# Kernel tuning notes

Hardware: AMD Instinct MI355X
Metric: run time of the kernel (lower is better)

## Reference

```python
import jax, jax.numpy as jnp
import numpy as np

INPUT_DIM = 20000
UNITS = 4096
NNZ = 2_000_000
BATCH = 2048


def setup_inputs() -> dict:
    key = jax.random.key(0)
    k1, k2, k3, k4 = jax.random.split(key, 4)
    x = jax.random.normal(k1, (BATCH, INPUT_DIM), dtype=jnp.float32)
    kernel_vector = jax.random.normal(k2, (NNZ,), dtype=jnp.float32) * 0.05
    bias = jnp.zeros((UNITS,), dtype=jnp.float32)
    rows = jax.random.randint(k3, (NNZ,), 0, INPUT_DIM, dtype=jnp.int32)
    cols = jax.random.randint(k4, (NNZ,), 0, UNITS, dtype=jnp.int32)
    nonzero_ind = jnp.stack([rows, cols], axis=1)  # (NNZ, 2)
    return {"x": x, "kernel_vector": kernel_vector, "bias": bias, "nonzero_ind": nonzero_ind}


def reference(x, kernel_vector, bias, nonzero_ind):
    # scatter_nd: build dense (input_dim, units) kernel from COO representation.
    # Duplicate indices accumulate (tf.scatter_nd semantics) -> use .add.
    trans = jnp.zeros((INPUT_DIM, UNITS), dtype=kernel_vector.dtype)
    trans = trans.at[nonzero_ind[:, 0], nonzero_ind[:, 1]].add(kernel_vector)
    out = x @ trans + bias  # (batch, units)
    return jnp.tanh(out)
```

## Files before the change

kernel.cpp:

```cpp
#include <hip/hip_runtime.h>
#include <cstdint>
#include <cstddef>

#define M_DIM 2048
#define N_DIM 4096
#define K_DIM 20000
#define KP    20480
#define KZ    10240
#define NTILE 160
#define WBT_BYTES  167772160UL
#define XB_OFFSET  167772160UL
#define CP_OFFSET  251658240UL
#define BIN_OFFSET CP_OFFSET
#define CUR_OFFSET 318767104UL
#define NBUCKET 256
#define BUCKET_CAP 16384
#define LDS_ECAP 9216

typedef __attribute__((ext_vector_type(8))) short short8;
typedef __attribute__((ext_vector_type(4))) float float4v;
typedef __attribute__((ext_vector_type(8))) unsigned short ushort8;

__device__ __forceinline__ unsigned short f2bf_rne(float f) {
    union { float f; unsigned int u; } v; v.f = f;
    unsigned int u = v.u;
    u += 0x7FFFu + ((u >> 16) & 1u);
    return (unsigned short)(u >> 16);
}

__device__ __forceinline__ void gload_lds16(const void* g, void* l) {
    __builtin_amdgcn_global_load_lds(
        (const __attribute__((address_space(1))) void*)g,
        (__attribute__((address_space(3))) void*)l, 16, 0, 0);
}

__global__ __launch_bounds__(256) void bin_kernel(
    const float* __restrict__ kv, const int* __restrict__ ind, int nnz,
    uint2* __restrict__ binned, unsigned int* __restrict__ cursor) {
    __shared__ unsigned int hist[NBUCKET];
    __shared__ unsigned int base[NBUCKET];
    __shared__ unsigned int run[NBUCKET];
    const int tid = threadIdx.x;
    const int per_block = (nnz + 1023) >> 10;
    const int start = blockIdx.x * per_block;
    const int limit = min(per_block, nnz - start);

    hist[tid] = 0u;
    __syncthreads();

    int bkt[8]; unsigned int meta[8]; float val[8];
    #pragma unroll
    for (int i = 0; i < 8; ++i) {
        int j = i * 256 + tid;
        bkt[i] = -1;
        if (j < limit) {
            int idx = start + j;
            int r = ind[2 * idx];
            int c = ind[2 * idx + 1];
            val[i] = kv[idx];
            bkt[i] = c >> 4;
            meta[i] = ((unsigned int)(c & 15) << 16) | (unsigned int)r;
            atomicAdd(&hist[bkt[i]], 1u);
        }
    }
    __syncthreads();
    {
        unsigned int n = hist[tid];
        base[tid] = n ? atomicAdd(&cursor[tid * 16], n) : 0u;
        run[tid] = 0u;
    }
    __syncthreads();
    #pragma unroll
    for (int i = 0; i < 8; ++i) {
        if (bkt[i] >= 0) {
            unsigned int slot = base[bkt[i]] + atomicAdd(&run[bkt[i]], 1u);
            if (slot < BUCKET_CAP) {
                uint2 e; e.x = meta[i]; e.y = __float_as_uint(val[i]);
                binned[(size_t)bkt[i] * BUCKET_CAP + slot] = e;
            }
        }
    }
}

__global__ __launch_bounds__(512) void accum_kernel(
    const uint2* __restrict__ binned, const unsigned int* __restrict__ cursor,
    unsigned short* __restrict__ Wbt) {
    __shared__ float row[KP];
    __shared__ uint2 ent[LDS_ECAP];
    const int b   = blockIdx.x;
    const int tid = threadIdx.x;
    const unsigned int count = min(cursor[b * 16], (unsigned int)BUCKET_CAP);
    const uint2* gsrc = binned + (size_t)b * BUCKET_CAP;

    for (unsigned int i = tid; i < count && i < LDS_ECAP; i += 512)
        ent[i] = gsrc[i];
    __syncthreads();

    for (int cc = 0; cc < 16; ++cc) {
        float4v* r4 = (float4v*)row;
        #pragma unroll
        for (int i = 0; i < 10; ++i)
            r4[tid + i * 512] = (float4v){0.f, 0.f, 0.f, 0.f};
        __syncthreads();
        for (unsigned int i = tid; i < count; i += 512) {
            uint2 e = (i < LDS_ECAP) ? ent[i] : gsrc[i];
            if ((int)(e.x >> 16) == cc)
                atomicAdd(&row[e.x & 0xFFFFu], __uint_as_float(e.y));
        }
        __syncthreads();
        unsigned short* dst = Wbt + (size_t)(b * 16 + cc) * KP;
        #pragma unroll
        for (int i = 0; i < 10; ++i) {
            int ch = tid + i * 512;
            float4v f = *(float4v*)&row[ch * 4];
            ushort4 o;
            o.x = f2bf_rne(f[0]); o.y = f2bf_rne(f[1]);
            o.z = f2bf_rne(f[2]); o.w = f2bf_rne(f[3]);
            *(ushort4*)(dst + ch * 4) = o;
        }
        __syncthreads();
    }
}

__global__ void convert_kernel(const float* __restrict__ src,
                               unsigned short* __restrict__ dst) {
    size_t t = (size_t)blockIdx.x * 256 + threadIdx.x;
    int row = (int)(t / 2560);
    int c8  = (int)(t % 2560);
    ushort8 o;
    if (c8 < 2500) {
        const float4* sv = (const float4*)(src + (size_t)row * K_DIM + (size_t)c8 * 8);
        float4 a = sv[0];
        float4 b = sv[1];
        o[0] = f2bf_rne(a.x); o[1] = f2bf_rne(a.y);
        o[2] = f2bf_rne(a.z); o[3] = f2bf_rne(a.w);
        o[4] = f2bf_rne(b.x); o[5] = f2bf_rne(b.y);
        o[6] = f2bf_rne(b.z); o[7] = f2bf_rne(b.w);
    } else {
        o = (ushort8)0;
    }
    *(ushort8*)(dst + (size_t)row * KP + (size_t)c8 * 8) = o;
}

__global__ __launch_bounds__(512, 2) void gemm256_kernel(
    const unsigned short* __restrict__ A,
    const unsigned short* __restrict__ Bt,
    float* __restrict__ Cp) {

    __shared__ unsigned short L[65536];

    const int t    = threadIdx.x;
    const int w    = t >> 6;
    const int l    = t & 63;
    const int quad = l >> 4;
    const int r16  = l & 15;
    const int wm   = w >> 2;
    const int wn   = w & 3;

    const int m0 = blockIdx.y * 256;
    const int n0 = blockIdx.x * 256;
    const size_t k0 = (size_t)blockIdx.z * KZ;

    const int lr8 = l >> 3;
    const int sl  = (l & 7) ^ lr8;
    const int w1024 = w << 10;

    const unsigned short* pA0 = A  + (size_t)(m0 +   0 + w * 8 + lr8) * KP + k0 + sl * 8;
    const unsigned short* pA1 = A  + (size_t)(m0 +  64 + w * 8 + lr8) * KP + k0 + sl * 8;
    const unsigned short* pA2 = A  + (size_t)(m0 + 128 + w * 8 + lr8) * KP + k0 + sl * 8;
    const unsigned short* pA3 = A  + (size_t)(m0 + 192 + w * 8 + lr8) * KP + k0 + sl * 8;
    const unsigned short* pB0 = Bt + (size_t)(n0 +   0 + w * 8 + lr8) * KP + k0 + sl * 8;
    const unsigned short* pB1 = Bt + (size_t)(n0 +  64 + w * 8 + lr8) * KP + k0 + sl * 8;
    const unsigned short* pB2 = Bt + (size_t)(n0 + 128 + w * 8 + lr8) * KP + k0 + sl * 8;
    const unsigned short* pB3 = Bt + (size_t)(n0 + 192 + w * 8 + lr8) * KP + k0 + sl * 8;

    char* Lb = (char*)L;

#define STG_A(OB, Q, P) do { \
    gload_lds16(P, Lb + (OB) + (Q) * 8192 + w1024); P += 64; } while (0)
#define STG_B(OB, Q, P) do { \
    gload_lds16(P, Lb + (OB) + 32768 + (Q) * 8192 + w1024); P += 64; } while (0)

    const int h   = r16 & 7;
    const int so0 = ((quad ^ h) << 4);
    const int so1 = (((4 | quad) ^ h) << 4);
    const int aoff = wm * 16384 + r16 * 128;
    const int boff = 32768 + wn * 8192 + r16 * 128;

    float4v acc[8][4];
#pragma unroll
    for (int i = 0; i < 8; ++i)
#pragma unroll
        for (int j = 0; j < 4; ++j)
            acc[i][j] = (float4v){0.f, 0.f, 0.f, 0.f};

    short8 bfr[4], af[4];

#define VM2 asm volatile("s_waitcnt vmcnt(2)" ::: "memory")
#define VMNONE ((void)0)

#define PHASE(BUF, MH, SO, LOADB, STG, VM) do { \
    const char* base_ = Lb + (BUF); \
    if (LOADB) { \
        _Pragma("unroll") \
        for (int j = 0; j < 4; ++j) \
            bfr[j] = *(const short8*)(base_ + boff + j * 2048 + (SO)); \
    } \
    _Pragma("unroll") \
    for (int i = 0; i < 4; ++i) \
        af[i] = *(const short8*)(base_ + aoff + (MH) * 8192 + i * 2048 + (SO)); \
    STG; \
    __builtin_amdgcn_s_barrier(); \
    asm volatile("s_waitcnt lgkmcnt(0)" ::: "memory"); \
    __builtin_amdgcn_s_setprio(1); \
    _Pragma("unroll") \
    for (int i = 0; i < 4; ++i) \
        _Pragma("unroll") \
        for (int j = 0; j < 4; ++j) \
            acc[(MH) * 4 + i][j] = __builtin_amdgcn_mfma_f32_16x16x32_bf16( \
                af[i], bfr[j], acc[(MH) * 4 + i][j], 0, 0, 0); \
    __builtin_amdgcn_s_setprio(0); \
    VM; \
    __builtin_amdgcn_s_barrier(); \
} while (0)

#define TILE(BUF, OB) do { \
    PHASE(BUF, 0, so0, true,  { STG_A(OB, 0, pA0); STG_A(OB, 1, pA1); }, VMNONE); \
    PHASE(BUF, 1, so0, false, { STG_A(OB, 2, pA2); STG_A(OB, 3, pA3); }, VMNONE); \
    PHASE(BUF, 0, so1, true,  { STG_B(OB, 2, pB2); STG_B(OB, 3, pB3); }, VMNONE); \
    PHASE(BUF, 1, so1, false, { STG_B(BUF, 0, pB0); STG_B(BUF, 1, pB1); }, VM2); \
} while (0)

    STG_A(0, 0, pA0); STG_A(0, 1, pA1); STG_A(0, 2, pA2); STG_A(0, 3, pA3);
    STG_B(0, 0, pB0); STG_B(0, 1, pB1); STG_B(0, 2, pB2); STG_B(0, 3, pB3);
    STG_B(65536, 0, pB0); STG_B(65536, 1, pB1);
    asm volatile("s_waitcnt vmcnt(2)" ::: "memory");
    __builtin_amdgcn_s_barrier();

#pragma unroll 1
    for (int it = 0; it < NTILE / 2; ++it) {
        TILE(0, 65536);
        TILE(65536, 0);
    }
    asm volatile("s_waitcnt vmcnt(0)" ::: "memory");

    float* Cz = Cp + (size_t)blockIdx.z * ((size_t)M_DIM * N_DIM);
#pragma unroll
    for (int i = 0; i < 8; ++i) {
        const int row = m0 + wm * 128 + i * 16 + quad * 4;
#pragma unroll
        for (int j = 0; j < 4; ++j) {
            const int col = n0 + wn * 64 + j * 16 + r16;
#pragma unroll
            for (int r = 0; r < 4; ++r)
                Cz[(size_t)(row + r) * N_DIM + col] = acc[i][j][r];
        }
    }
#undef TILE
#undef PHASE
#undef STG_A
#undef STG_B
#undef VM2
#undef VMNONE
}

__global__ void combine_kernel(const float* __restrict__ Cp,
                               const float* __restrict__ bias,
                               float* __restrict__ out) {
    size_t t = (size_t)blockIdx.x * 256 + threadIdx.x;
    const size_t stride = (size_t)M_DIM * N_DIM / 4;
    float4 a = ((const float4*)Cp)[t];
    float4 b = ((const float4*)Cp)[t + stride];
    float4 bv = ((const float4*)bias)[t & (N_DIM / 4 - 1)];
    float4 o;
    o.x = tanhf(a.x + b.x + bv.x);
    o.y = tanhf(a.y + b.y + bv.y);
    o.z = tanhf(a.z + b.z + bv.z);
    o.w = tanhf(a.w + b.w + bv.w);
    ((float4*)out)[t] = o;
}

extern "C" void kernel_launch(void* const* d_in, const int* in_sizes, int n_in,
                              void* d_out, int out_size, void* d_ws, size_t ws_size,
                              hipStream_t stream) {
    const float* x    = (const float*)d_in[0];
    const float* kv   = (const float*)d_in[1];
    const float* bias = (const float*)d_in[2];
    const int*   ind  = (const int*)d_in[3];
    const int nnz = in_sizes[1];

    unsigned short* Wbt = (unsigned short*)d_ws;
    unsigned short* xb  = (unsigned short*)((char*)d_ws + XB_OFFSET);
    float* Cp           = (float*)((char*)d_ws + CP_OFFSET);
    uint2* binned       = (uint2*)((char*)d_ws + BIN_OFFSET);
    unsigned int* cursor = (unsigned int*)((char*)d_ws + CUR_OFFSET);

    hipMemsetAsync(cursor, 0, NBUCKET * 64, stream);
    bin_kernel<<<1024, 256, 0, stream>>>(kv, ind, nnz, binned, cursor);
    accum_kernel<<<NBUCKET, 512, 0, stream>>>(binned, cursor, Wbt);
    convert_kernel<<<(M_DIM * (KP / 8)) / 256, 256, 0, stream>>>(x, xb);
    gemm256_kernel<<<dim3(N_DIM / 256, M_DIM / 256, 2), 512, 0, stream>>>(
        xb, Wbt, Cp);
    combine_kernel<<<(M_DIM * N_DIM) / (256 * 4), 256, 0, stream>>>(
        Cp, bias, (float*)d_out);
}
```

Before: 613.9 us.

## Fuse x conversion into binning kernel and split accum buckets across two blocks

The bf16 conversion of x is merged into the COO binning kernel as extra blocks, which removes one launch and lets the conversion run alongside binning. The accumulation kernel now launches two blocks per bucket, each handling 8 of the 16 columns, which doubles the grid from 256 to 512 blocks on a GPU with many CUs. The LDS staging of bucket entries is dropped, so each block rereads its bucket from global memory once per column pass.

```diff
diff --git a/kernel.cpp b/kernel.cpp
--- a/kernel.cpp
+++ b/kernel.cpp
@@ -15,7 +15,8 @@
 #define CUR_OFFSET 318767104UL
 #define NBUCKET 256
 #define BUCKET_CAP 16384
-#define LDS_ECAP 9216
+#define BIN_BLOCKS 1024
+#define CONV_BLOCKS 20480
 
 typedef __attribute__((ext_vector_type(8))) short short8;
 typedef __attribute__((ext_vector_type(4))) float float4v;
@@ -34,81 +35,101 @@
         (__attribute__((address_space(3))) void*)l, 16, 0, 0);
 }
 
-__global__ __launch_bounds__(256) void bin_kernel(
+__global__ __launch_bounds__(256) void prep_kernel(
     const float* __restrict__ kv, const int* __restrict__ ind, int nnz,
-    uint2* __restrict__ binned, unsigned int* __restrict__ cursor) {
+    uint2* __restrict__ binned, unsigned int* __restrict__ cursor,
+    const float* __restrict__ x, unsigned short* __restrict__ xb) {
     __shared__ unsigned int hist[NBUCKET];
     __shared__ unsigned int base[NBUCKET];
     __shared__ unsigned int run[NBUCKET];
     const int tid = threadIdx.x;
-    const int per_block = (nnz + 1023) >> 10;
-    const int start = blockIdx.x * per_block;
-    const int limit = min(per_block, nnz - start);
-
-    hist[tid] = 0u;
-    __syncthreads();
-
-    int bkt[8]; unsigned int meta[8]; float val[8];
-    #pragma unroll
-    for (int i = 0; i < 8; ++i) {
-        int j = i * 256 + tid;
-        bkt[i] = -1;
-        if (j < limit) {
-            int idx = start + j;
-            int r = ind[2 * idx];
-            int c = ind[2 * idx + 1];
-            val[i] = kv[idx];
-            bkt[i] = c >> 4;
-            meta[i] = ((unsigned int)(c & 15) << 16) | (unsigned int)r;
-            atomicAdd(&hist[bkt[i]], 1u);
-        }
-    }
-    __syncthreads();
-    {
-        unsigned int n = hist[tid];
-        base[tid] = n ? atomicAdd(&cursor[tid * 16], n) : 0u;
-        run[tid] = 0u;
-    }
-    __syncthreads();
-    #pragma unroll
-    for (int i = 0; i < 8; ++i) {
-        if (bkt[i] >= 0) {
-            unsigned int slot = base[bkt[i]] + atomicAdd(&run[bkt[i]], 1u);
-            if (slot < BUCKET_CAP) {
-                uint2 e; e.x = meta[i]; e.y = __float_as_uint(val[i]);
-                binned[(size_t)bkt[i] * BUCKET_CAP + slot] = e;
+
+    if (blockIdx.x < BIN_BLOCKS) {
+        const int per_block = (nnz + BIN_BLOCKS - 1) / BIN_BLOCKS;
+        const int start = blockIdx.x * per_block;
+        const int limit = min(per_block, nnz - start);
+
+        hist[tid] = 0u;
+        __syncthreads();
+
+        int bkt[8]; unsigned int meta[8]; float val[8];
+        #pragma unroll
+        for (int i = 0; i < 8; ++i) {
+            int j = i * 256 + tid;
+            bkt[i] = -1;
+            if (j < limit) {
+                int idx = start + j;
+                int r = ind[2 * idx];
+                int c = ind[2 * idx + 1];
+                val[i] = kv[idx];
+                bkt[i] = c >> 4;
+                meta[i] = ((unsigned int)(c & 15) << 16) | (unsigned int)r;
+                atomicAdd(&hist[bkt[i]], 1u);
             }
         }
-    }
+        __syncthreads();
+        {
+            unsigned int n = hist[tid];
+            base[tid] = n ? atomicAdd(&cursor[tid * 16], n) : 0u;
+            run[tid] = 0u;
+        }
+        __syncthreads();
+        #pragma unroll
+        for (int i = 0; i < 8; ++i) {
+            if (bkt[i] >= 0) {
+                unsigned int slot = base[bkt[i]] + atomicAdd(&run[bkt[i]], 1u);
+                if (slot < BUCKET_CAP) {
+                    uint2 e; e.x = meta[i]; e.y = __float_as_uint(val[i]);
+                    binned[(size_t)bkt[i] * BUCKET_CAP + slot] = e;
+                }
+            }
+        }
+        return;
+    }
+
+    size_t t = (size_t)(blockIdx.x - BIN_BLOCKS) * 256 + tid;
+    int row = (int)(t / 2560);
+    int c8  = (int)(t % 2560);
+    ushort8 o;
+    if (c8 < 2500) {
+        const float4* sv = (const float4*)(x + (size_t)row * K_DIM + (size_t)c8 * 8);
+        float4 a = sv[0];
+        float4 b = sv[1];
+        o[0] = f2bf_rne(a.x); o[1] = f2bf_rne(a.y);
+        o[2] = f2bf_rne(a.z); o[3] = f2bf_rne(a.w);
+        o[4] = f2bf_rne(b.x); o[5] = f2bf_rne(b.y);
+        o[6] = f2bf_rne(b.z); o[7] = f2bf_rne(b.w);
+    } else {
+        o = (ushort8)0;
+    }
+    *(ushort8*)(xb + (size_t)row * KP + (size_t)c8 * 8) = o;
 }
 
 __global__ __launch_bounds__(512) void accum_kernel(
     const uint2* __restrict__ binned, const unsigned int* __restrict__ cursor,
     unsigned short* __restrict__ Wbt) {
     __shared__ float row[KP];
-    __shared__ uint2 ent[LDS_ECAP];
-    const int b   = blockIdx.x;
-    const int tid = threadIdx.x;
-    const unsigned int count = min(cursor[b * 16], (unsigned int)BUCKET_CAP);
-    const uint2* gsrc = binned + (size_t)b * BUCKET_CAP;
-
-    for (unsigned int i = tid; i < count && i < LDS_ECAP; i += 512)
-        ent[i] = gsrc[i];
-    __syncthreads();
-
-    for (int cc = 0; cc < 16; ++cc) {
+    const int b      = blockIdx.x;
+    const int bucket = b >> 1;
+    const int half   = b & 1;
+    const int tid    = threadIdx.x;
+    const unsigned int count = min(cursor[bucket * 16], (unsigned int)BUCKET_CAP);
+    const uint2* gsrc = binned + (size_t)bucket * BUCKET_CAP;
+
+    for (int cc = 0; cc < 8; ++cc) {
+        const int colLow = half * 8 + cc;
         float4v* r4 = (float4v*)row;
         #pragma unroll
         for (int i = 0; i < 10; ++i)
             r4[tid + i * 512] = (float4v){0.f, 0.f, 0.f, 0.f};
         __syncthreads();
         for (unsigned int i = tid; i < count; i += 512) {
-            uint2 e = (i < LDS_ECAP) ? ent[i] : gsrc[i];
-            if ((int)(e.x >> 16) == cc)
+            uint2 e = gsrc[i];
+            if ((int)(e.x >> 16) == colLow)
                 atomicAdd(&row[e.x & 0xFFFFu], __uint_as_float(e.y));
         }
         __syncthreads();
-        unsigned short* dst = Wbt + (size_t)(b * 16 + cc) * KP;
+        unsigned short* dst = Wbt + (size_t)(bucket * 16 + colLow) * KP;
         #pragma unroll
         for (int i = 0; i < 10; ++i) {
             int ch = tid + i * 512;
@@ -120,26 +141,6 @@
         }
         __syncthreads();
     }
-}
-
-__global__ void convert_kernel(const float* __restrict__ src,
-                               unsigned short* __restrict__ dst) {
-    size_t t = (size_t)blockIdx.x * 256 + threadIdx.x;
-    int row = (int)(t / 2560);
-    int c8  = (int)(t % 2560);
-    ushort8 o;
-    if (c8 < 2500) {
-        const float4* sv = (const float4*)(src + (size_t)row * K_DIM + (size_t)c8 * 8);
-        float4 a = sv[0];
-        float4 b = sv[1];
-        o[0] = f2bf_rne(a.x); o[1] = f2bf_rne(a.y);
-        o[2] = f2bf_rne(a.z); o[3] = f2bf_rne(a.w);
-        o[4] = f2bf_rne(b.x); o[5] = f2bf_rne(b.y);
-        o[6] = f2bf_rne(b.z); o[7] = f2bf_rne(b.w);
-    } else {
-        o = (ushort8)0;
-    }
-    *(ushort8*)(dst + (size_t)row * KP + (size_t)c8 * 8) = o;
 }
 
 __global__ __launch_bounds__(512, 2) void gemm256_kernel(
@@ -296,9 +297,9 @@
     unsigned int* cursor = (unsigned int*)((char*)d_ws + CUR_OFFSET);
 
     hipMemsetAsync(cursor, 0, NBUCKET * 64, stream);
-    bin_kernel<<<1024, 256, 0, stream>>>(kv, ind, nnz, binned, cursor);
-    accum_kernel<<<NBUCKET, 512, 0, stream>>>(binned, cursor, Wbt);
-    convert_kernel<<<(M_DIM * (KP / 8)) / 256, 256, 0, stream>>>(x, xb);
+    prep_kernel<<<BIN_BLOCKS + CONV_BLOCKS, 256, 0, stream>>>(
+        kv, ind, nnz, binned, cursor, x, xb);
+    accum_kernel<<<512, 512, 0, stream>>>(binned, cursor, Wbt);
     gemm256_kernel<<<dim3(N_DIM / 256, M_DIM / 256, 2), 512, 0, stream>>>(
         xb, Wbt, Cp);
     combine_kernel<<<(M_DIM * N_DIM) / (256 * 4), 256, 0, stream>>>(
```

After: 617.5 us. Within noise of the previous version (+0.6%).
